# Kernel optimization log

Hardware: AMD Instinct MI355X
Metric: run time of the kernel (lower is better)

## Reference

```python
import jax, jax.numpy as jnp
import numpy as np

B, S, D, H = 2, 2048, 1024, 16
DK = D // H


def setup_inputs() -> dict:
    key = jax.random.key(0)
    ks = jax.random.split(key, 7)
    x = jax.random.normal(ks[0], (B, S, D), dtype=jnp.float32)
    gamma = jax.random.normal(ks[1], (D,), dtype=jnp.float32)
    mask = jax.random.randint(ks[2], (B, S), 0, 2, dtype=jnp.int32)
    w_qkv_w = jax.random.normal(ks[3], (D, 3 * D), dtype=jnp.float32) / np.sqrt(D)
    w_qkv_b = jax.random.normal(ks[4], (3 * D,), dtype=jnp.float32) * 0.02
    w_o_w = jax.random.normal(ks[5], (D, D), dtype=jnp.float32) / np.sqrt(D)
    w_o_b = jax.random.normal(ks[6], (D,), dtype=jnp.float32) * 0.02
    return {"x": x, "gamma": gamma, "mask": mask, "w_qkv_w": w_qkv_w,
            "w_qkv_b": w_qkv_b, "w_o_w": w_o_w, "w_o_b": w_o_b}


def reference(x, gamma, mask, w_qkv_w, w_qkv_b, w_o_w, w_o_b):
    b, s, d = x.shape
    # QKV projection, then per-head interleaved chunk (matches torch view+chunk)
    qkv = x @ w_qkv_w + w_qkv_b                      # [B,S,3D]
    qkv = qkv.reshape(b, s, H, 3 * DK).transpose(0, 2, 1, 3)  # [B,H,S,3*dk]
    q, k, v = jnp.split(qkv, 3, axis=-1)             # each [B,H,S,dk]
    scale = 1.0 / np.sqrt(DK).astype(np.float32)
    scores = jnp.einsum('bhqd,bhkd->bhqk', q, k) * scale  # [B,H,S,S]
    m = mask[:, None, None, :]                       # 2D mask -> [B,1,1,S]
    scores = jnp.where(m == 0, -jnp.inf, scores)
    attn = jax.nn.softmax(scores, axis=-1)           # dropout p=0.0 -> identity
    out = jnp.einsum('bhqk,bhkd->bhqd', attn, v)     # [B,H,S,dk]
    out = out.transpose(0, 2, 1, 3).reshape(b, s, d) # [B,S,D]
    out = out @ w_o_w + w_o_b
    return (gamma + 1.0) * out
```

## Files before the change

kernel.cpp:

```cpp
#include <hip/hip_runtime.h>
#include <hip/hip_bf16.h>


using bf16 = __hip_bfloat16;
typedef __attribute__((ext_vector_type(8))) short bf16x8;
typedef __attribute__((ext_vector_type(4))) short bf16x4;
typedef __attribute__((ext_vector_type(4))) float f32x4;

#define QSCALE 0.18033688011112042f

static __device__ __forceinline__ f32x4 mfma_bf16(bf16x8 a, bf16x8 b, f32x4 c) {
    return __builtin_amdgcn_mfma_f32_16x16x32_bf16(a, b, c, 0, 0, 0);
}

static __device__ __forceinline__ void gld_lds16(const void* g, void* s) {
    __builtin_amdgcn_global_load_lds(
        (const __attribute__((address_space(1))) unsigned int*)g,
        (__attribute__((address_space(3))) unsigned int*)s,
        16, 0, 0);
}

static __device__ __forceinline__ short f2s(float f) {
    bf16 h = __float2bfloat16(f);
    return *reinterpret_cast<short*>(&h);
}

__global__ void cast_bf16_kernel(const float* __restrict__ in, bf16* __restrict__ out, int n4) {
    int i = blockIdx.x * blockDim.x + threadIdx.x;
    if (i >= n4) return;
    float4 f = reinterpret_cast<const float4*>(in)[i];
    out[4*i+0] = __float2bfloat16(f.x);
    out[4*i+1] = __float2bfloat16(f.y);
    out[4*i+2] = __float2bfloat16(f.z);
    out[4*i+3] = __float2bfloat16(f.w);
}

__global__ void transpose_cast_kernel(const float* __restrict__ in, bf16* __restrict__ out,
                                      int R, int C) {
    __shared__ float tile[32][33];
    int c0 = blockIdx.x * 32, r0 = blockIdx.y * 32;
    int x = threadIdx.x, y = threadIdx.y;
#pragma unroll
    for (int i = 0; i < 32; i += 8) tile[y + i][x] = in[(size_t)(r0 + y + i) * C + c0 + x];
    __syncthreads();
#pragma unroll
    for (int i = 0; i < 32; i += 8)
        out[(size_t)(c0 + y + i) * R + r0 + x] = __float2bfloat16(tile[x][y + i]);
}

__global__ void transpose_v_kernel(const bf16* __restrict__ in, bf16* __restrict__ out) {
    __shared__ bf16 t[64][72];
    const int bh = blockIdx.y, s0 = blockIdx.x * 64;
    const int r = threadIdx.x >> 2, c16 = (threadIdx.x & 3) * 16;
    const uint4* src = (const uint4*)(in + ((size_t)bh * 2048 + s0 + r) * 64 + c16);
    uint4 a = src[0], b = src[1];
    *(uint4*)&t[r][c16] = a;
    *(uint4*)&t[r][c16 + 8] = b;
    __syncthreads();
    bf16 tmp[16];
#pragma unroll
    for (int i = 0; i < 16; ++i) tmp[i] = t[c16 + i][r];
    uint4* dst = (uint4*)(out + ((size_t)bh * 64 + r) * 2048 + s0 + c16);
    dst[0] = ((uint4*)tmp)[0];
    dst[1] = ((uint4*)tmp)[1];
}

template <int EPI>
__global__ __launch_bounds__(256, 2)
void gemm_bt_kernel(const bf16* __restrict__ A, const bf16* __restrict__ Bt,
                    int M, int N, int K,
                    const float* __restrict__ bias, const float* __restrict__ gamma,
                    bf16* __restrict__ Qout, bf16* __restrict__ Kout, bf16* __restrict__ Vout,
                    float* __restrict__ Cout) {
    __shared__ __align__(16) bf16 As[128 * 64];
    __shared__ __align__(16) bf16 Bs[128 * 64];

    const int tid  = threadIdx.x;
    const int wave = tid >> 6, lane = tid & 63;
    const int quad = lane >> 4, l16 = lane & 15;
    const int wr = wave >> 1, wc = wave & 1;
    const int bm = blockIdx.y, bn = blockIdx.x;

    f32x4 acc[4][4] = {};

    const int crow = lane >> 3;
    const int sblk = (lane & 7) ^ (crow & 7);
    const bf16* gA[4]; const bf16* gB[4]; bf16* lA[4]; bf16* lB[4];
#pragma unroll
    for (int c = 0; c < 4; ++c) {
        int rt = wave * 32 + c * 8 + crow;
        gA[c] = A  + (size_t)(bm * 128 + rt) * K + sblk * 8;
        gB[c] = Bt + (size_t)(bn * 128 + rt) * K + sblk * 8;
        lA[c] = As + (wave * 4 + c) * 512 + lane * 8;
        lB[c] = Bs + (wave * 4 + c) * 512 + lane * 8;
    }
    const int xr = l16 & 7;

    for (int k0 = 0; k0 < K; k0 += 64) {
#pragma unroll
        for (int c = 0; c < 4; ++c) gld_lds16(gA[c] + k0, lA[c]);
#pragma unroll
        for (int c = 0; c < 4; ++c) gld_lds16(gB[c] + k0, lB[c]);
        __syncthreads();
#pragma unroll
        for (int ks = 0; ks < 2; ++ks) {
            bf16x8 af[4], bfr[4];
#pragma unroll
            for (int mi = 0; mi < 4; ++mi)
                af[mi] = *(const bf16x8*)(As + (wr * 64 + mi * 16 + l16) * 64 + ((4 * ks + quad) ^ xr) * 8);
#pragma unroll
            for (int ni = 0; ni < 4; ++ni)
                bfr[ni] = *(const bf16x8*)(Bs + (wc * 64 + ni * 16 + l16) * 64 + ((4 * ks + quad) ^ xr) * 8);
#pragma unroll
            for (int mi = 0; mi < 4; ++mi)
#pragma unroll
                for (int ni = 0; ni < 4; ++ni)
                    acc[mi][ni] = mfma_bf16(af[mi], bfr[ni], acc[mi][ni]);
        }
        __syncthreads();
    }

#pragma unroll
    for (int mi = 0; mi < 4; ++mi) {
#pragma unroll
        for (int ni = 0; ni < 4; ++ni) {
#pragma unroll
            for (int r = 0; r < 4; ++r) {
                int row = bm * 128 + wr * 64 + mi * 16 + quad * 4 + r;
                int col = bn * 128 + wc * 64 + ni * 16 + l16;
                float v = acc[mi][ni][r];
                if (EPI == 0) {
                    v += bias[col];
                    int h = col / 192;
                    int rr = col - h * 192;
                    int which = rr >> 6, dk = rr & 63;
                    int b = row >> 11, s = row & 2047;
                    size_t bh = (size_t)b * 16 + h;
                    if (which == 0) {
                        Qout[(bh * 2048 + s) * 64 + dk] = __float2bfloat16(v * QSCALE);
                    } else if (which == 1) {
                        Kout[(bh * 2048 + s) * 64 + dk] = __float2bfloat16(v);
                    } else {
                        Vout[(bh * 2048 + s) * 64 + dk] = __float2bfloat16(v);
                    }
                } else {
                    float o = (gamma[col] + 1.0f) * (v + bias[col]);
                    Cout[(size_t)row * N + col] = o;
                }
            }
        }
    }
}

__global__ __launch_bounds__(256, 2)
void attn_kernel(const bf16* __restrict__ Qb, const bf16* __restrict__ Kb,
                 const bf16* __restrict__ Vt, const int* __restrict__ mask,
                 bf16* __restrict__ Aout) {
    __shared__ __align__(16) bf16 Ks[64 * 72];
    __shared__ __align__(16) bf16 Vs[64 * 76];
    __shared__ __align__(16) float Biass[64];

    const int bh = blockIdx.y;
    const int b = bh >> 4, h = bh & 15;
    const int q0 = blockIdx.x * 128;
    const int tid = threadIdx.x;
    const int wave = tid >> 6, lane = tid & 63;
    const int quad = lane >> 4, l16 = lane & 15;

    bf16x8 aq[2][2];
#pragma unroll
    for (int m = 0; m < 2; ++m) {
        const bf16* qp = Qb + ((size_t)bh * 2048 + q0 + wave * 32 + m * 16 + l16) * 64;
        aq[m][0] = *(const bf16x8*)(qp + quad * 8);
        aq[m][1] = *(const bf16x8*)(qp + 32 + quad * 8);
    }

    bf16x8 ones;
#pragma unroll
    for (int j = 0; j < 8; ++j) ones[j] = (short)0x3F80;

    f32x4 O[2][4] = {};
    f32x4 Lacc[2] = {};

    const int srow = tid >> 2, spart = tid & 3;
    const bf16* gK = Kb + ((size_t)bh * 2048 + srow) * 64 + spart * 16;
    const bf16* gV = Vt + ((size_t)bh * 64 + srow) * 2048 + spart * 16;
    uint4* lK = (uint4*)(Ks + srow * 72 + spart * 16);
    uint4* lV = (uint4*)(Vs + srow * 76 + spart * 16);

    uint4 kr0, kr1, vr0, vr1; int mreg = 1;
    {
        const uint4* nk = (const uint4*)gK;
        const uint4* nv = (const uint4*)gV;
        kr0 = nk[0]; kr1 = nk[1];
        vr0 = nv[0]; vr1 = nv[1];
        if (tid < 64) mreg = mask[b * 2048 + tid];
    }

    for (int kt = 0; kt < 32; ++kt) {
        lK[0] = kr0; lK[1] = kr1;
        lV[0] = vr0; lV[1] = vr1;
        if (tid < 64) Biass[tid] = mreg ? -24.0f : -1e30f;
        __syncthreads();

        if (kt + 1 < 32) {
            const uint4* nk = (const uint4*)(gK + (size_t)(kt + 1) * 64 * 64);
            const uint4* nv = (const uint4*)(gV + (kt + 1) * 64);
            kr0 = nk[0]; kr1 = nk[1];
            vr0 = nv[0]; vr1 = nv[1];
            if (tid < 64) mreg = mask[b * 2048 + (kt + 1) * 64 + tid];
        }

        f32x4 bias4[4];
        bf16x8 bk[4][2];
#pragma unroll
        for (int kt4 = 0; kt4 < 4; ++kt4) {
            bias4[kt4] = *(const f32x4*)(Biass + kt4 * 16 + quad * 4);
            const bf16* kp = Ks + (kt4 * 16 + l16) * 72 + quad * 8;
            bk[kt4][0] = *(const bf16x8*)kp;
            bk[kt4][1] = *(const bf16x8*)(kp + 32);
        }
        bf16x8 bv8[2][4];
#pragma unroll
        for (int a = 0; a < 2; ++a) {
#pragma unroll
            for (int nt = 0; nt < 4; ++nt) {
                const bf16* vp = Vs + (nt * 16 + l16) * 76 + a * 32 + quad * 4;
                bf16x4 lo = *(const bf16x4*)vp;
                bf16x4 hi = *(const bf16x4*)(vp + 16);
                bf16x8 f;
                f[0] = lo[0]; f[1] = lo[1]; f[2] = lo[2]; f[3] = lo[3];
                f[4] = hi[0]; f[5] = hi[1]; f[6] = hi[2]; f[7] = hi[3];
                bv8[a][nt] = f;
            }
        }

#pragma unroll
        for (int m = 0; m < 2; ++m) {
            f32x4 sv[4];
#pragma unroll
            for (int kt4 = 0; kt4 < 4; ++kt4) {
                f32x4 c = {0.f, 0.f, 0.f, 0.f};
                c = mfma_bf16(bk[kt4][0], aq[m][0], c);
                c = mfma_bf16(bk[kt4][1], aq[m][1], c);
                sv[kt4] = c;
            }
            float p[4][4];
#pragma unroll
            for (int kt4 = 0; kt4 < 4; ++kt4)
#pragma unroll
                for (int r = 0; r < 4; ++r)
                    p[kt4][r] = __builtin_amdgcn_exp2f(sv[kt4][r] + bias4[kt4][r]);

#pragma unroll
            for (int a = 0; a < 2; ++a) {
                bf16x8 pa;
                pa[0] = f2s(p[2*a][0]);   pa[1] = f2s(p[2*a][1]);
                pa[2] = f2s(p[2*a][2]);   pa[3] = f2s(p[2*a][3]);
                pa[4] = f2s(p[2*a+1][0]); pa[5] = f2s(p[2*a+1][1]);
                pa[6] = f2s(p[2*a+1][2]); pa[7] = f2s(p[2*a+1][3]);
                Lacc[m] = mfma_bf16(pa, ones, Lacc[m]);
#pragma unroll
                for (int nt = 0; nt < 4; ++nt)
                    O[m][nt] = mfma_bf16(pa, bv8[a][nt], O[m][nt]);
            }
        }
        __syncthreads();
    }

#pragma unroll
    for (int m = 0; m < 2; ++m) {
        float inv[4];
#pragma unroll
        for (int r = 0; r < 4; ++r) inv[r] = __builtin_amdgcn_rcpf(Lacc[m][r]);
#pragma unroll
        for (int nt = 0; nt < 4; ++nt) {
#pragma unroll
            for (int r = 0; r < 4; ++r) {
                int row = q0 + wave * 32 + m * 16 + quad * 4 + r;
                Aout[((size_t)b * 2048 + row) * 1024 + h * 64 + nt * 16 + l16] =
                    __float2bfloat16(O[m][nt][r] * inv[r]);
            }
        }
    }
}

extern "C" void kernel_launch(void* const* d_in, const int* in_sizes, int n_in,
                              void* d_out, int out_size, void* d_ws, size_t ws_size,
                              hipStream_t stream) {
    const float* x     = (const float*)d_in[0];
    const float* gamma = (const float*)d_in[1];
    const int*   mask  = (const int*)d_in[2];
    const float* wqkv  = (const float*)d_in[3];
    const float* bqkv  = (const float*)d_in[4];
    const float* wo    = (const float*)d_in[5];
    const float* bo    = (const float*)d_in[6];
    float* out = (float*)d_out;

    char* ws = (char*)d_ws;
    const size_t MB = 1u << 20;
    bf16* xb    = (bf16*)(ws);
    bf16* wqkvT = (bf16*)(ws + 8 * MB);
    bf16* woT   = (bf16*)(ws + 14 * MB);
    bf16* Qb    = (bf16*)(ws + 16 * MB);
    bf16* Kb    = (bf16*)(ws + 24 * MB);
    bf16* Vt    = (bf16*)(ws + 32 * MB);
    bf16* Vtmp  = (bf16*)(ws + 40 * MB);
    bf16* attn  = (bf16*)(ws + 40 * MB);

    cast_bf16_kernel<<<4096, 256, 0, stream>>>(x, xb, 4194304 / 4);
    transpose_cast_kernel<<<dim3(96, 32), dim3(32, 8), 0, stream>>>(wqkv, wqkvT, 1024, 3072);
    transpose_cast_kernel<<<dim3(32, 32), dim3(32, 8), 0, stream>>>(wo, woT, 1024, 1024);

    gemm_bt_kernel<0><<<dim3(24, 32), 256, 0, stream>>>(
        xb, wqkvT, 4096, 3072, 1024, bqkv, nullptr, Qb, Kb, Vtmp, nullptr);

    transpose_v_kernel<<<dim3(32, 32), 256, 0, stream>>>(Vtmp, Vt);

    attn_kernel<<<dim3(16, 32), 256, 0, stream>>>(Qb, Kb, Vt, mask, attn);

    gemm_bt_kernel<1><<<dim3(8, 32), 256, 0, stream>>>(
        attn, woT, 4096, 1024, 1024, bo, gamma, nullptr, nullptr, nullptr, out);
}
```

Baseline: 209.4 us.

## Double-buffer attention K/V tiles and retile output GEMM for more blocks

```diff
diff --git a/kernel.cpp b/kernel.cpp
--- a/kernel.cpp
+++ b/kernel.cpp
@@ -65,14 +65,16 @@
     dst[1] = ((uint4*)tmp)[1];
 }
 
-template <int EPI>
-__global__ __launch_bounds__(256, 2)
+template <int EPI, int TM, int MINW>
+__global__ __launch_bounds__(256, MINW)
 void gemm_bt_kernel(const bf16* __restrict__ A, const bf16* __restrict__ Bt,
                     int M, int N, int K,
                     const float* __restrict__ bias, const float* __restrict__ gamma,
                     bf16* __restrict__ Qout, bf16* __restrict__ Kout, bf16* __restrict__ Vout,
                     float* __restrict__ Cout) {
-    __shared__ __align__(16) bf16 As[128 * 64];
+    constexpr int MI = TM / 32;
+    constexpr int CA = TM / 32;
+    __shared__ __align__(16) bf16 As[TM * 64];
     __shared__ __align__(16) bf16 Bs[128 * 64];
 
     const int tid  = threadIdx.x;
@@ -81,38 +83,42 @@
     const int wr = wave >> 1, wc = wave & 1;
     const int bm = blockIdx.y, bn = blockIdx.x;
 
-    f32x4 acc[4][4] = {};
+    f32x4 acc[MI][4] = {};
 
     const int crow = lane >> 3;
     const int sblk = (lane & 7) ^ (crow & 7);
-    const bf16* gA[4]; const bf16* gB[4]; bf16* lA[4]; bf16* lB[4];
+    const bf16* gA[CA]; const bf16* gB[4]; bf16* lA[CA]; bf16* lB[4];
+#pragma unroll
+    for (int c = 0; c < CA; ++c) {
+        int ch = wave * CA + c;
+        gA[c] = A + (size_t)(bm * TM + ch * 8 + crow) * K + sblk * 8;
+        lA[c] = As + ch * 512 + lane * 8;
+    }
 #pragma unroll
     for (int c = 0; c < 4; ++c) {
-        int rt = wave * 32 + c * 8 + crow;
-        gA[c] = A  + (size_t)(bm * 128 + rt) * K + sblk * 8;
-        gB[c] = Bt + (size_t)(bn * 128 + rt) * K + sblk * 8;
-        lA[c] = As + (wave * 4 + c) * 512 + lane * 8;
-        lB[c] = Bs + (wave * 4 + c) * 512 + lane * 8;
+        int ch = wave * 4 + c;
+        gB[c] = Bt + (size_t)(bn * 128 + ch * 8 + crow) * K + sblk * 8;
+        lB[c] = Bs + ch * 512 + lane * 8;
     }
     const int xr = l16 & 7;
 
     for (int k0 = 0; k0 < K; k0 += 64) {
 #pragma unroll
-        for (int c = 0; c < 4; ++c) gld_lds16(gA[c] + k0, lA[c]);
+        for (int c = 0; c < CA; ++c) gld_lds16(gA[c] + k0, lA[c]);
 #pragma unroll
         for (int c = 0; c < 4; ++c) gld_lds16(gB[c] + k0, lB[c]);
         __syncthreads();
 #pragma unroll
         for (int ks = 0; ks < 2; ++ks) {
-            bf16x8 af[4], bfr[4];
-#pragma unroll
-            for (int mi = 0; mi < 4; ++mi)
-                af[mi] = *(const bf16x8*)(As + (wr * 64 + mi * 16 + l16) * 64 + ((4 * ks + quad) ^ xr) * 8);
+            bf16x8 af[MI], bfr[4];
+#pragma unroll
+            for (int mi = 0; mi < MI; ++mi)
+                af[mi] = *(const bf16x8*)(As + (wr * (TM/2) + mi * 16 + l16) * 64 + ((4 * ks + quad) ^ xr) * 8);
 #pragma unroll
             for (int ni = 0; ni < 4; ++ni)
                 bfr[ni] = *(const bf16x8*)(Bs + (wc * 64 + ni * 16 + l16) * 64 + ((4 * ks + quad) ^ xr) * 8);
 #pragma unroll
-            for (int mi = 0; mi < 4; ++mi)
+            for (int mi = 0; mi < MI; ++mi)
 #pragma unroll
                 for (int ni = 0; ni < 4; ++ni)
                     acc[mi][ni] = mfma_bf16(af[mi], bfr[ni], acc[mi][ni]);
@@ -121,12 +127,12 @@
     }
 
 #pragma unroll
-    for (int mi = 0; mi < 4; ++mi) {
+    for (int mi = 0; mi < MI; ++mi) {
 #pragma unroll
         for (int ni = 0; ni < 4; ++ni) {
 #pragma unroll
             for (int r = 0; r < 4; ++r) {
-                int row = bm * 128 + wr * 64 + mi * 16 + quad * 4 + r;
+                int row = bm * TM + wr * (TM/2) + mi * 16 + quad * 4 + r;
                 int col = bn * 128 + wc * 64 + ni * 16 + l16;
                 float v = acc[mi][ni][r];
                 if (EPI == 0) {
@@ -156,9 +162,9 @@
 void attn_kernel(const bf16* __restrict__ Qb, const bf16* __restrict__ Kb,
                  const bf16* __restrict__ Vt, const int* __restrict__ mask,
                  bf16* __restrict__ Aout) {
-    __shared__ __align__(16) bf16 Ks[64 * 72];
-    __shared__ __align__(16) bf16 Vs[64 * 76];
-    __shared__ __align__(16) float Biass[64];
+    __shared__ __align__(16) bf16 Ks[2][64 * 72];
+    __shared__ __align__(16) bf16 Vs[2][64 * 76];
+    __shared__ __align__(16) float Biass[2][64];
 
     const int bh = blockIdx.y;
     const int b = bh >> 4, h = bh & 15;
@@ -185,38 +191,50 @@
     const int srow = tid >> 2, spart = tid & 3;
     const bf16* gK = Kb + ((size_t)bh * 2048 + srow) * 64 + spart * 16;
     const bf16* gV = Vt + ((size_t)bh * 64 + srow) * 2048 + spart * 16;
-    uint4* lK = (uint4*)(Ks + srow * 72 + spart * 16);
-    uint4* lV = (uint4*)(Vs + srow * 76 + spart * 16);
+    uint4* lK[2]; uint4* lV[2];
+#pragma unroll
+    for (int p = 0; p < 2; ++p) {
+        lK[p] = (uint4*)(Ks[p] + srow * 72 + spart * 16);
+        lV[p] = (uint4*)(Vs[p] + srow * 76 + spart * 16);
+    }
 
     uint4 kr0, kr1, vr0, vr1; int mreg = 1;
     {
         const uint4* nk = (const uint4*)gK;
         const uint4* nv = (const uint4*)gV;
-        kr0 = nk[0]; kr1 = nk[1];
-        vr0 = nv[0]; vr1 = nv[1];
+        kr0 = nk[0]; kr1 = nk[1]; vr0 = nv[0]; vr1 = nv[1];
         if (tid < 64) mreg = mask[b * 2048 + tid];
+        lK[0][0] = kr0; lK[0][1] = kr1;
+        lV[0][0] = vr0; lV[0][1] = vr1;
+        if (tid < 64) Biass[0][tid] = mreg ? -24.0f : -1e30f;
+        const uint4* nk1 = (const uint4*)(gK + 4096);
+        const uint4* nv1 = (const uint4*)(gV + 64);
+        kr0 = nk1[0]; kr1 = nk1[1]; vr0 = nv1[0]; vr1 = nv1[1];
+        if (tid < 64) mreg = mask[b * 2048 + 64 + tid];
     }
 
     for (int kt = 0; kt < 32; ++kt) {
-        lK[0] = kr0; lK[1] = kr1;
-        lV[0] = vr0; lV[1] = vr1;
-        if (tid < 64) Biass[tid] = mreg ? -24.0f : -1e30f;
         __syncthreads();
+        const int cur = kt & 1, nxt = cur ^ 1;
 
         if (kt + 1 < 32) {
-            const uint4* nk = (const uint4*)(gK + (size_t)(kt + 1) * 64 * 64);
-            const uint4* nv = (const uint4*)(gV + (kt + 1) * 64);
-            kr0 = nk[0]; kr1 = nk[1];
-            vr0 = nv[0]; vr1 = nv[1];
-            if (tid < 64) mreg = mask[b * 2048 + (kt + 1) * 64 + tid];
+            lK[nxt][0] = kr0; lK[nxt][1] = kr1;
+            lV[nxt][0] = vr0; lV[nxt][1] = vr1;
+            if (tid < 64) Biass[nxt][tid] = mreg ? -24.0f : -1e30f;
+        }
+        if (kt + 2 < 32) {
+            const uint4* nk = (const uint4*)(gK + (size_t)(kt + 2) * 4096);
+            const uint4* nv = (const uint4*)(gV + (kt + 2) * 64);
+            kr0 = nk[0]; kr1 = nk[1]; vr0 = nv[0]; vr1 = nv[1];
+            if (tid < 64) mreg = mask[b * 2048 + (kt + 2) * 64 + tid];
         }
 
         f32x4 bias4[4];
         bf16x8 bk[4][2];
 #pragma unroll
         for (int kt4 = 0; kt4 < 4; ++kt4) {
-            bias4[kt4] = *(const f32x4*)(Biass + kt4 * 16 + quad * 4);
-            const bf16* kp = Ks + (kt4 * 16 + l16) * 72 + quad * 8;
+            bias4[kt4] = *(const f32x4*)(&Biass[cur][0] + kt4 * 16 + quad * 4);
+            const bf16* kp = Ks[cur] + (kt4 * 16 + l16) * 72 + quad * 8;
             bk[kt4][0] = *(const bf16x8*)kp;
             bk[kt4][1] = *(const bf16x8*)(kp + 32);
         }
@@ -225,7 +243,7 @@
         for (int a = 0; a < 2; ++a) {
 #pragma unroll
             for (int nt = 0; nt < 4; ++nt) {
-                const bf16* vp = Vs + (nt * 16 + l16) * 76 + a * 32 + quad * 4;
+                const bf16* vp = Vs[cur] + (nt * 16 + l16) * 76 + a * 32 + quad * 4;
                 bf16x4 lo = *(const bf16x4*)vp;
                 bf16x4 hi = *(const bf16x4*)(vp + 16);
                 bf16x8 f;
@@ -265,7 +283,6 @@
                     O[m][nt] = mfma_bf16(pa, bv8[a][nt], O[m][nt]);
             }
         }
-        __syncthreads();
     }
 
 #pragma unroll
@@ -312,13 +329,13 @@
     transpose_cast_kernel<<<dim3(96, 32), dim3(32, 8), 0, stream>>>(wqkv, wqkvT, 1024, 3072);
     transpose_cast_kernel<<<dim3(32, 32), dim3(32, 8), 0, stream>>>(wo, woT, 1024, 1024);
 
-    gemm_bt_kernel<0><<<dim3(24, 32), 256, 0, stream>>>(
+    gemm_bt_kernel<0, 128, 3><<<dim3(24, 32), 256, 0, stream>>>(
         xb, wqkvT, 4096, 3072, 1024, bqkv, nullptr, Qb, Kb, Vtmp, nullptr);
 
     transpose_v_kernel<<<dim3(32, 32), 256, 0, stream>>>(Vtmp, Vt);
 
     attn_kernel<<<dim3(16, 32), 256, 0, stream>>>(Qb, Kb, Vt, mask, attn);
 
-    gemm_bt_kernel<1><<<dim3(8, 32), 256, 0, stream>>>(
+    gemm_bt_kernel<1, 64, 4><<<dim3(8, 64), 256, 0, stream>>>(
         attn, woT, 4096, 1024, 1024, bo, gamma, nullptr, nullptr, nullptr, out);
 }
```

Result: faster. 195.0 us (-6.9%).
